# Kernel tuning notes

Hardware: AMD Instinct MI355X
Metric: run time of the kernel (lower is better)

## Reference

```python
import jax, jax.numpy as jnp
import numpy as np

N_NODES = 50000
N_EDGES = 800000
NUM_GRAPHS = 256
EPS = 1e-5


def _gcn_conv(x, edge_index, W, b):
    # PyG GCNConv: add self-loops, sym-normalize, aggregate, then add bias.
    n = x.shape[0]
    xw = x @ W  # [N, out]
    loops = jnp.arange(n)
    row = jnp.concatenate([edge_index[0], loops])  # source
    col = jnp.concatenate([edge_index[1], loops])  # target
    deg = jax.ops.segment_sum(jnp.ones_like(col, dtype=xw.dtype), col, num_segments=n)
    dinv = jnp.where(deg > 0, jax.lax.rsqrt(deg), 0.0)
    norm = dinv[row] * dinv[col]  # [E+N]
    msg = norm[:, None] * xw[row]  # gather + scale
    out = jax.ops.segment_sum(msg, col, num_segments=n)  # scatter-add
    return out + b


def _bn(x, g, b, m, v):
    # inference-mode batch norm
    return (x - m) * jax.lax.rsqrt(v + EPS) * g + b


def reference(x, edge_index, batch, gcn_W0, gcn_b0, bn_g0, bn_b0, bn_m0, bn_v0,
              gcn_W1, gcn_b1, bn_g1, bn_b1, bn_m1, bn_v1,
              hW1, hb1, hg1, hbb1, hm1, hv1,
              hW2, hb2, hg2, hbb2, hm2, hv2,
              hW3, hb3, hW4, hb4):
    # GCN block 0
    h = _gcn_conv(x, edge_index, gcn_W0, gcn_b0)
    h = jax.nn.relu(_bn(h, bn_g0, bn_b0, bn_m0, bn_v0))  # dropout = identity (eval)
    # GCN block 1
    h = _gcn_conv(h, edge_index, gcn_W1, gcn_b1)
    h = jax.nn.relu(_bn(h, bn_g1, bn_b1, bn_m1, bn_v1))
    # global mean pool over graphs
    sums = jax.ops.segment_sum(h, batch, num_segments=NUM_GRAPHS)
    cnts = jax.ops.segment_sum(jnp.ones_like(batch, dtype=h.dtype), batch, num_segments=NUM_GRAPHS)
    pooled = sums / jnp.maximum(cnts, 1.0)[:, None]  # [G, 64]
    # MLP head (eval: dropout identity)
    z = jax.nn.relu(_bn(pooled @ hW1 + hb1, hg1, hbb1, hm1, hv1))
    z = jax.nn.relu(_bn(z @ hW2 + hb2, hg2, hbb2, hm2, hv2))
    z = jax.nn.relu(z @ hW3 + hb3)
    out = (z @ hW4 + hb4).reshape(-1)  # [G]
    return out


def setup_inputs() -> dict:
    key = jax.random.key(0)
    ks = jax.random.split(key, 12)
    d = 64
    inp = {
        'x': jax.random.normal(ks[0], (N_NODES, d), dtype=jnp.float32),
        'edge_index': jax.random.randint(ks[1], (2, N_EDGES), 0, N_NODES, dtype=jnp.int64),
        'batch': jnp.sort(jax.random.randint(ks[2], (N_NODES,), 0, NUM_GRAPHS, dtype=jnp.int64)),
        'gcn_W0': jax.random.normal(ks[3], (d, d), dtype=jnp.float32) * 0.1,
        'gcn_b0': jnp.zeros((d,), jnp.float32),
        'bn_g0': jnp.ones((d,), jnp.float32), 'bn_b0': jnp.zeros((d,), jnp.float32),
        'bn_m0': jnp.zeros((d,), jnp.float32), 'bn_v0': jnp.ones((d,), jnp.float32),
        'gcn_W1': jax.random.normal(ks[4], (d, d), dtype=jnp.float32) * 0.1,
        'gcn_b1': jnp.zeros((d,), jnp.float32),
        'bn_g1': jnp.ones((d,), jnp.float32), 'bn_b1': jnp.zeros((d,), jnp.float32),
        'bn_m1': jnp.zeros((d,), jnp.float32), 'bn_v1': jnp.ones((d,), jnp.float32),
        'hW1': jax.random.normal(ks[5], (d, 256), dtype=jnp.float32) * 0.1,
        'hb1': jnp.zeros((256,), jnp.float32),
        'hg1': jnp.ones((256,), jnp.float32), 'hbb1': jnp.zeros((256,), jnp.float32),
        'hm1': jnp.zeros((256,), jnp.float32), 'hv1': jnp.ones((256,), jnp.float32),
        'hW2': jax.random.normal(ks[6], (256, 128), dtype=jnp.float32) * 0.1,
        'hb2': jnp.zeros((128,), jnp.float32),
        'hg2': jnp.ones((128,), jnp.float32), 'hbb2': jnp.zeros((128,), jnp.float32),
        'hm2': jnp.zeros((128,), jnp.float32), 'hv2': jnp.ones((128,), jnp.float32),
        'hW3': jax.random.normal(ks[7], (128, 64), dtype=jnp.float32) * 0.1,
        'hb3': jnp.zeros((64,), jnp.float32),
        'hW4': jax.random.normal(ks[8], (64, 1), dtype=jnp.float32) * 0.1,
        'hb4': jnp.zeros((1,), jnp.float32),
    }
    return inp
```

## Files before the change

kernel.cpp:

```cpp
#include <hip/hip_runtime.h>
#include <hip/hip_bf16.h>
#include <hip/hip_fp16.h>

#define N_NODES 50000
#define N_EDGES 800000
#define NUM_GRAPHS 256
#define D 64
#define EPS 1e-5f
#define N_PART 8
#define PART_SIZE (N_NODES / N_PART)
#define SCAT_CHUNKS 512
#define WP 72

typedef _Float16 half8_t __attribute__((ext_vector_type(8)));
typedef float f32x4 __attribute__((ext_vector_type(4)));

__global__ __launch_bounds__(256) void scatter_cnt_kernel(
        const int* __restrict__ ei, int* __restrict__ cnt,
        unsigned short* __restrict__ ssrc, int cap, int E) {
    int p     = blockIdx.x & (N_PART - 1);
    int chunk = blockIdx.x >> 3;
    int per   = (E + SCAT_CHUNKS - 1) / SCAT_CHUNKS;
    int lo    = chunk * per;
    int hi    = lo + per; if (hi > E) hi = E;
    for (int e = lo + threadIdx.x; e < hi; e += 256) {
        int c = ei[E + e];
        if (c / PART_SIZE == p) {
            int r = ei[e];
            int pos = atomicAdd(&cnt[c], 1);
            if (pos < cap) ssrc[(size_t)c * cap + pos] = (unsigned short)r;
        }
    }
}

__global__ __launch_bounds__(256) void gemm64_kernel(const float* __restrict__ X,
                                                     const float* __restrict__ W,
                                                     const int* __restrict__ cnt,
                                                     __half* __restrict__ Yh, int N) {
    __shared__ _Float16 Xs[64 * WP];
    __shared__ _Float16 Wt[64 * WP];
    int tid  = threadIdx.x;
    int base = blockIdx.x * 64;
    for (int i = tid; i < 4096; i += 256) {
        int k = i >> 6, n = i & 63;
        Wt[n * WP + k] = (_Float16)W[i];
    }
    for (int i = tid; i < 1024; i += 256) {
        int r = i >> 4, c4 = (i & 15) * 4;
        float4 xv = (base + r < N)
            ? ((const float4*)X)[(size_t)(base + r) * 16 + (i & 15)]
            : make_float4(0.f, 0.f, 0.f, 0.f);
        _Float16* dst = &Xs[r * WP + c4];
        dst[0] = (_Float16)xv.x; dst[1] = (_Float16)xv.y;
        dst[2] = (_Float16)xv.z; dst[3] = (_Float16)xv.w;
    }
    __syncthreads();
    int wave  = tid >> 6;
    int lane  = tid & 63;
    int m     = lane & 15;
    int q     = lane >> 4;
    int row16 = wave * 16;
    half8_t a0 = *(const half8_t*)&Xs[(row16 + m) * WP + q * 8];
    half8_t a1 = *(const half8_t*)&Xs[(row16 + m) * WP + 32 + q * 8];
    f32x4 acc[4];
#pragma unroll
    for (int ct = 0; ct < 4; ct++) {
        half8_t b0 = *(const half8_t*)&Wt[(ct * 16 + m) * WP + q * 8];
        half8_t b1 = *(const half8_t*)&Wt[(ct * 16 + m) * WP + 32 + q * 8];
        f32x4 c = {0.f, 0.f, 0.f, 0.f};
        c = __builtin_amdgcn_mfma_f32_16x16x32_f16(a0, b0, c, 0, 0, 0);
        c = __builtin_amdgcn_mfma_f32_16x16x32_f16(a1, b1, c, 0, 0, 0);
        acc[ct] = c;
    }
    int   rows[4];
    float ws[4];
#pragma unroll
    for (int reg = 0; reg < 4; reg++) {
        rows[reg] = base + row16 + q * 4 + reg;
        ws[reg] = (rows[reg] < N) ? rsqrtf((float)cnt[rows[reg]] + 1.0f) : 0.0f;
    }
#pragma unroll
    for (int ct = 0; ct < 4; ct++) {
#pragma unroll
        for (int reg = 0; reg < 4; reg++) {
            if (rows[reg] < N)
                Yh[(size_t)rows[reg] * 64 + ct * 16 + m] =
                    (__half)(ws[reg] * acc[ct][reg]);
        }
    }
}

__global__ __launch_bounds__(256) void agg_bn_kernel(
        const __half* __restrict__ xwh, const int* __restrict__ cnt,
        const unsigned short* __restrict__ ssrc, int cap,
        const float* __restrict__ b, const float* __restrict__ g,
        const float* __restrict__ bb, const float* __restrict__ m,
        const float* __restrict__ var,
        float* __restrict__ out, int N) {
    int wave = (blockIdx.x * blockDim.x + threadIdx.x) >> 6;
    int lane = threadIdx.x & 63;
    if (wave >= N) return;
    int c   = wave;
    int sub = lane >> 3;
    int f2  = lane & 7;
    const uint4* xw8 = (const uint4*)xwh;
    int n = cnt[c];
    if (n > cap) n = cap;
    size_t base = (size_t)c * cap;
    float dc = rsqrtf((float)n + 1.0f);
    float4 accA = make_float4(0.f, 0.f, 0.f, 0.f);
    float4 accB = accA;
    if (sub == 0) {
        uint4 v = xw8[(size_t)c * 8 + f2];
        __half2* hp = (__half2*)&v;
        float2 q0 = __half22float2(hp[0]), q1 = __half22float2(hp[1]);
        float2 q2 = __half22float2(hp[2]), q3 = __half22float2(hp[3]);
        accA.x = q0.x; accA.y = q0.y; accA.z = q1.x; accA.w = q1.y;
        accB.x = q2.x; accB.y = q2.y; accB.z = q3.x; accB.w = q3.y;
    }
    for (int e0 = 0; e0 < n; e0 += 8) {
        int e = e0 + sub;
        if (e < n) {
            int r = (int)ssrc[base + e];
            uint4 v = xw8[(size_t)r * 8 + f2];
            __half2* hp = (__half2*)&v;
            float2 q0 = __half22float2(hp[0]), q1 = __half22float2(hp[1]);
            float2 q2 = __half22float2(hp[2]), q3 = __half22float2(hp[3]);
            accA.x += q0.x; accA.y += q0.y;
            accA.z += q1.x; accA.w += q1.y;
            accB.x += q2.x; accB.y += q2.y;
            accB.z += q3.x; accB.w += q3.y;
        }
    }
#pragma unroll
    for (int off = 8; off < 64; off <<= 1) {
        accA.x += __shfl_xor(accA.x, off, 64); accA.y += __shfl_xor(accA.y, off, 64);
        accA.z += __shfl_xor(accA.z, off, 64); accA.w += __shfl_xor(accA.w, off, 64);
        accB.x += __shfl_xor(accB.x, off, 64); accB.y += __shfl_xor(accB.y, off, 64);
        accB.z += __shfl_xor(accB.z, off, 64); accB.w += __shfl_xor(accB.w, off, 64);
    }
    if (sub < 2) {
        int i4 = 2 * f2 + sub;
        float4 acc = sub ? accB : accA;
        float4 b4  = ((const float4*)b)[i4];
        float4 m4  = ((const float4*)m)[i4];
        float4 v4_ = ((const float4*)var)[i4];
        float4 g4  = ((const float4*)g)[i4];
        float4 bb4 = ((const float4*)bb)[i4];
        float4 h;
        h.x = (acc.x * dc + b4.x - m4.x) * (1.0f / sqrtf(v4_.x + EPS)) * g4.x + bb4.x;
        h.y = (acc.y * dc + b4.y - m4.y) * (1.0f / sqrtf(v4_.y + EPS)) * g4.y + bb4.y;
        h.z = (acc.z * dc + b4.z - m4.z) * (1.0f / sqrtf(v4_.z + EPS)) * g4.z + bb4.z;
        h.w = (acc.w * dc + b4.w - m4.w) * (1.0f / sqrtf(v4_.w + EPS)) * g4.w + bb4.w;
        h.x = h.x > 0.f ? h.x : 0.f;
        h.y = h.y > 0.f ? h.y : 0.f;
        h.z = h.z > 0.f ? h.z : 0.f;
        h.w = h.w > 0.f ? h.w : 0.f;
        ((float4*)out)[(size_t)c * 16 + i4] = h;
    }
}

__global__ __launch_bounds__(256) void pool_head_kernel(
        const float* __restrict__ h, const int* __restrict__ batch,
        const float* __restrict__ hW1, const float* __restrict__ hb1,
        const float* __restrict__ hg1, const float* __restrict__ hbb1,
        const float* __restrict__ hm1, const float* __restrict__ hv1,
        const float* __restrict__ hW2, const float* __restrict__ hb2,
        const float* __restrict__ hg2, const float* __restrict__ hbb2,
        const float* __restrict__ hm2, const float* __restrict__ hv2,
        const float* __restrict__ hW3, const float* __restrict__ hb3,
        const float* __restrict__ hW4, const float* __restrict__ hb4,
        float* __restrict__ out) {
    __shared__ int se[2];
    __shared__ float red[256];
    __shared__ float pooled[64];
    __shared__ float z1[256];
    __shared__ float z2[128];
    __shared__ float z3[64];
    int g = blockIdx.x;
    int t = threadIdx.x;
    if (t < 2) {
        int target = g + t;
        int lo = 0, hi = N_NODES;
        while (lo < hi) {
            int mid = (lo + hi) >> 1;
            if (batch[mid] < target) lo = mid + 1; else hi = mid;
        }
        se[t] = lo;
    }
    __syncthreads();
    int start = se[0], end = se[1];
    {
        int f = t & 63, rg = t >> 6;
        float part = 0.0f;
        for (int r = start + rg; r < end; r += 4) part += h[(size_t)r * 64 + f];
        red[t] = part;
        __syncthreads();
        if (t < 64) {
            float s = red[t] + red[t + 64] + red[t + 128] + red[t + 192];
            float cnt = (float)(end - start);
            cnt = cnt > 1.0f ? cnt : 1.0f;
            pooled[t] = s / cnt;
        }
    }
    __syncthreads();
    {
        float acc = hb1[t];
#pragma unroll
        for (int k = 0; k < 64; k++) acc += pooled[k] * hW1[k * 256 + t];
        acc = (acc - hm1[t]) * (1.0f / sqrtf(hv1[t] + EPS)) * hg1[t] + hbb1[t];
        z1[t] = acc > 0.0f ? acc : 0.0f;
    }
    __syncthreads();
    if (t < 128) {
        float acc = hb2[t];
#pragma unroll 8
        for (int k = 0; k < 256; k++) acc += z1[k] * hW2[k * 128 + t];
        acc = (acc - hm2[t]) * (1.0f / sqrtf(hv2[t] + EPS)) * hg2[t] + hbb2[t];
        z2[t] = acc > 0.0f ? acc : 0.0f;
    }
    __syncthreads();
    if (t < 64) {
        float acc = hb3[t];
#pragma unroll 8
        for (int k = 0; k < 128; k++) acc += z2[k] * hW3[k * 64 + t];
        z3[t] = acc > 0.0f ? acc : 0.0f;
    }
    __syncthreads();
    if (t < 64) {
        float v = z3[t] * hW4[t];
        for (int off = 32; off > 0; off >>= 1) v += __shfl_down(v, off, 64);
        if (t == 0) out[g] = v + hb4[0];
    }
}

extern "C" void kernel_launch(void* const* d_in, const int* in_sizes, int n_in,
                              void* d_out, int out_size, void* d_ws, size_t ws_size,
                              hipStream_t stream) {
    const float* x     = (const float*)d_in[0];
    const int*   ei    = (const int*)d_in[1];
    const int*   batch = (const int*)d_in[2];
    const float* W0 = (const float*)d_in[3];
    const float* b0 = (const float*)d_in[4];
    const float* g0 = (const float*)d_in[5];
    const float* bb0 = (const float*)d_in[6];
    const float* m0 = (const float*)d_in[7];
    const float* v0 = (const float*)d_in[8];
    const float* W1 = (const float*)d_in[9];
    const float* b1 = (const float*)d_in[10];
    const float* g1 = (const float*)d_in[11];
    const float* bb1 = (const float*)d_in[12];
    const float* m1 = (const float*)d_in[13];
    const float* v1 = (const float*)d_in[14];
    const float* hW1 = (const float*)d_in[15];
    const float* hb1 = (const float*)d_in[16];
    const float* hg1 = (const float*)d_in[17];
    const float* hbb1 = (const float*)d_in[18];
    const float* hm1 = (const float*)d_in[19];
    const float* hv1 = (const float*)d_in[20];
    const float* hW2 = (const float*)d_in[21];
    const float* hb2 = (const float*)d_in[22];
    const float* hg2 = (const float*)d_in[23];
    const float* hbb2 = (const float*)d_in[24];
    const float* hm2 = (const float*)d_in[25];
    const float* hv2 = (const float*)d_in[26];
    const float* hW3 = (const float*)d_in[27];
    const float* hb3 = (const float*)d_in[28];
    const float* hW4 = (const float*)d_in[29];
    const float* hb4 = (const float*)d_in[30];
    float* out = (float*)d_out;

    float*  bufA = (float*)d_ws;
    __half* xwh  = (__half*)bufA;
    float*  bufB = bufA + (size_t)N_NODES * D;
    int*    cnt  = (int*)(bufB + (size_t)N_NODES * D);
    unsigned short* ssrc = (unsigned short*)(cnt + N_NODES);

    size_t used  = ((size_t)2 * N_NODES * D + N_NODES) * 4;
    int cap = 64;
    if (ws_size >= used) {
        size_t avail = (ws_size - used) / ((size_t)N_NODES * 2);
        if (avail < (size_t)cap) cap = (int)avail & ~7;
    } else {
        cap = 0;
    }

    const int NT = 256;
    hipMemsetAsync(cnt, 0, (size_t)N_NODES * 4, stream);

    scatter_cnt_kernel<<<SCAT_CHUNKS * N_PART, NT, 0, stream>>>(ei, cnt, ssrc, cap, N_EDGES);

    gemm64_kernel<<<(N_NODES + 63) / 64, NT, 0, stream>>>(x, W0, cnt, xwh, N_NODES);
    agg_bn_kernel<<<(N_NODES * 64 + NT - 1) / NT, NT, 0, stream>>>(
        xwh, cnt, ssrc, cap, b0, g0, bb0, m0, v0, bufB, N_NODES);

    gemm64_kernel<<<(N_NODES + 63) / 64, NT, 0, stream>>>(bufB, W1, cnt, xwh, N_NODES);
    agg_bn_kernel<<<(N_NODES * 64 + NT - 1) / NT, NT, 0, stream>>>(
        xwh, cnt, ssrc, cap, b1, g1, bb1, m1, v1, bufB, N_NODES);

    pool_head_kernel<<<NUM_GRAPHS, NT, 0, stream>>>(bufB, batch,
        hW1, hb1, hg1, hbb1, hm1, hv1,
        hW2, hb2, hg2, hbb2, hm2, hv2,
        hW3, hb3, hW4, hb4, out);
}
```

Baseline: 265.7 us.

## Map eight target nodes per wave in aggregation and unroll gathers by four

The aggregation kernel now assigns one 8-lane group per target node, so each wave handles eight nodes instead of one. This removes the cross-lane shuffle reduction and the idle lanes that appeared when a node had few neighbors. Each group reads four 16-bit source indices at once and issues four independent row gathers, giving more memory-level parallelism. In exchange, each lane walks a node's whole neighbor list serially. The vectorized uint2 index read assumes cap is a multiple of 4 and can read up to three padding entries past n, which are masked out.

```diff
diff --git a/kernel.cpp b/kernel.cpp
--- a/kernel.cpp
+++ b/kernel.cpp
@@ -90,6 +90,14 @@
     }
 }
 
+__device__ __forceinline__ void acc_row(uint4 v, float4& A, float4& B) {
+    __half2* hp = (__half2*)&v;
+    float2 q0 = __half22float2(hp[0]), q1 = __half22float2(hp[1]);
+    float2 q2 = __half22float2(hp[2]), q3 = __half22float2(hp[3]);
+    A.x += q0.x; A.y += q0.y; A.z += q1.x; A.w += q1.y;
+    B.x += q2.x; B.y += q2.y; B.z += q3.x; B.w += q3.y;
+}
+
 __global__ __launch_bounds__(256) void agg_bn_kernel(
         const __half* __restrict__ xwh, const int* __restrict__ cnt,
         const unsigned short* __restrict__ ssrc, int cap,
@@ -97,51 +105,39 @@
         const float* __restrict__ bb, const float* __restrict__ m,
         const float* __restrict__ var,
         float* __restrict__ out, int N) {
-    int wave = (blockIdx.x * blockDim.x + threadIdx.x) >> 6;
+    int gid  = blockIdx.x * blockDim.x + threadIdx.x;
     int lane = threadIdx.x & 63;
-    if (wave >= N) return;
-    int c   = wave;
-    int sub = lane >> 3;
-    int f2  = lane & 7;
+    int wave = gid >> 6;
+    int grp  = lane >> 3;
+    int f2   = lane & 7;
+    int c = wave * 8 + grp;
+    if (c >= N) return;
     const uint4* xw8 = (const uint4*)xwh;
     int n = cnt[c];
     if (n > cap) n = cap;
-    size_t base = (size_t)c * cap;
     float dc = rsqrtf((float)n + 1.0f);
     float4 accA = make_float4(0.f, 0.f, 0.f, 0.f);
     float4 accB = accA;
-    if (sub == 0) {
-        uint4 v = xw8[(size_t)c * 8 + f2];
-        __half2* hp = (__half2*)&v;
-        float2 q0 = __half22float2(hp[0]), q1 = __half22float2(hp[1]);
-        float2 q2 = __half22float2(hp[2]), q3 = __half22float2(hp[3]);
-        accA.x = q0.x; accA.y = q0.y; accA.z = q1.x; accA.w = q1.y;
-        accB.x = q2.x; accB.y = q2.y; accB.z = q3.x; accB.w = q3.y;
-    }
-    for (int e0 = 0; e0 < n; e0 += 8) {
-        int e = e0 + sub;
-        if (e < n) {
-            int r = (int)ssrc[base + e];
-            uint4 v = xw8[(size_t)r * 8 + f2];
-            __half2* hp = (__half2*)&v;
-            float2 q0 = __half22float2(hp[0]), q1 = __half22float2(hp[1]);
-            float2 q2 = __half22float2(hp[2]), q3 = __half22float2(hp[3]);
-            accA.x += q0.x; accA.y += q0.y;
-            accA.z += q1.x; accA.w += q1.y;
-            accB.x += q2.x; accB.y += q2.y;
-            accB.z += q3.x; accB.w += q3.y;
-        }
-    }
-#pragma unroll
-    for (int off = 8; off < 64; off <<= 1) {
-        accA.x += __shfl_xor(accA.x, off, 64); accA.y += __shfl_xor(accA.y, off, 64);
-        accA.z += __shfl_xor(accA.z, off, 64); accA.w += __shfl_xor(accA.w, off, 64);
-        accB.x += __shfl_xor(accB.x, off, 64); accB.y += __shfl_xor(accB.y, off, 64);
-        accB.z += __shfl_xor(accB.z, off, 64); accB.w += __shfl_xor(accB.w, off, 64);
-    }
-    if (sub < 2) {
-        int i4 = 2 * f2 + sub;
-        float4 acc = sub ? accB : accA;
+    acc_row(xw8[(size_t)c * 8 + f2], accA, accB);
+    const unsigned short* idx = &ssrc[(size_t)c * cap];
+    const uint4 z4 = make_uint4(0, 0, 0, 0);
+    for (int e0 = 0; e0 < n; e0 += 4) {
+        uint2 i4 = *(const uint2*)&idx[e0];
+        int r0 = i4.x & 0xffff, r1 = i4.x >> 16;
+        int r2 = i4.y & 0xffff, r3 = i4.y >> 16;
+        uint4 v0 = (e0 + 0 < n) ? xw8[(size_t)r0 * 8 + f2] : z4;
+        uint4 v1 = (e0 + 1 < n) ? xw8[(size_t)r1 * 8 + f2] : z4;
+        uint4 v2 = (e0 + 2 < n) ? xw8[(size_t)r2 * 8 + f2] : z4;
+        uint4 v3 = (e0 + 3 < n) ? xw8[(size_t)r3 * 8 + f2] : z4;
+        acc_row(v0, accA, accB);
+        acc_row(v1, accA, accB);
+        acc_row(v2, accA, accB);
+        acc_row(v3, accA, accB);
+    }
+#pragma unroll
+    for (int half = 0; half < 2; half++) {
+        int i4 = 2 * f2 + half;
+        float4 acc = half ? accB : accA;
         float4 b4  = ((const float4*)b)[i4];
         float4 m4  = ((const float4*)m)[i4];
         float4 v4_ = ((const float4*)var)[i4];
@@ -290,12 +286,13 @@
 
     scatter_cnt_kernel<<<SCAT_CHUNKS * N_PART, NT, 0, stream>>>(ei, cnt, ssrc, cap, N_EDGES);
 
+    int agg_blocks = ((N_NODES + 7) / 8 * 64 + NT - 1) / NT;
     gemm64_kernel<<<(N_NODES + 63) / 64, NT, 0, stream>>>(x, W0, cnt, xwh, N_NODES);
-    agg_bn_kernel<<<(N_NODES * 64 + NT - 1) / NT, NT, 0, stream>>>(
+    agg_bn_kernel<<<agg_blocks, NT, 0, stream>>>(
         xwh, cnt, ssrc, cap, b0, g0, bb0, m0, v0, bufB, N_NODES);
 
     gemm64_kernel<<<(N_NODES + 63) / 64, NT, 0, stream>>>(bufB, W1, cnt, xwh, N_NODES);
-    agg_bn_kernel<<<(N_NODES * 64 + NT - 1) / NT, NT, 0, stream>>>(
+    agg_bn_kernel<<<agg_blocks, NT, 0, stream>>>(
         xwh, cnt, ssrc, cap, b1, g1, bb1, m1, v1, bufB, N_NODES);
 
     pool_head_kernel<<<NUM_GRAPHS, NT, 0, stream>>>(bufB, batch,
```

Result: no change. 267.6 us (+0.7%).
